# Performance work log

Hardware: AMD Instinct MI355X
Metric: run time of the kernel (lower is better)

The kernel has to match this reference:

```python
import jax, jax.numpy as jnp
import numpy as np
import math

N = 10000      # nodes (batched protein residues)
E = 160000     # edges (avg degree 16)
D = 1280       # node/hidden dim (ESM2-650M)
M = 24         # message_dim
EE = 16        # edge_embedding_dim (sinusoidal distance features)
L = 6          # num EGNN layers
LN_EPS = 1e-5


def setup_inputs() -> dict:
    key = jax.random.key(0)
    ks = jax.random.split(key, 20)
    s = 0.02
    h = jax.random.normal(ks[0], (N, D), jnp.float32)
    pos = jax.random.normal(ks[1], (N, 3), jnp.float32) * 10.0
    edge_index = jax.random.randint(ks[2], (2, E), 0, N, jnp.int32)
    msg_in_dim = 2 * D + EE + 1  # h_i, h_j, edge_attr, radial
    params = dict(
        node_emb_W=jax.random.normal(ks[3], (D, D), jnp.float32) * s,
        node_emb_b=jnp.zeros((D,), jnp.float32),
        msg_W1=jax.random.normal(ks[4], (L, msg_in_dim, M), jnp.float32) * s,
        msg_b1=jnp.zeros((L, M), jnp.float32),
        msg_W2=jax.random.normal(ks[5], (L, M, M), jnp.float32) * s,
        msg_b2=jnp.zeros((L, M), jnp.float32),
        coord_W1=jax.random.normal(ks[6], (L - 1, M, M), jnp.float32) * s,
        coord_b1=jnp.zeros((L - 1, M), jnp.float32),
        coord_W2=jax.random.normal(ks[7], (L - 1, M, 1), jnp.float32) * s,  # no bias
        node_W1=jax.random.normal(ks[8], (L, D + M, M), jnp.float32) * s,
        node_b1=jnp.zeros((L, M), jnp.float32),
        node_W2=jax.random.normal(ks[9], (L, M, D), jnp.float32) * s,
        node_b2=jnp.zeros((L, D), jnp.float32),
        ln_g=jnp.ones((L, D), jnp.float32),
        ln_b=jnp.zeros((L, D), jnp.float32),
    )
    return dict(h=h, pos=pos, edge_index=edge_index, **params)


def reference(h, pos, edge_index, node_emb_W, node_emb_b, msg_W1, msg_b1,
              msg_W2, msg_b2, coord_W1, coord_b1, coord_W2,
              node_W1, node_b1, node_W2, node_b2, ln_g, ln_b):
    row, col = edge_index[0], edge_index[1]  # PyG: row=source j, col=target i

    # sinusoidal distance embedding from initial coordinates (computed once)
    freqs = jnp.exp(-math.log(10000.0) * jnp.arange(0, EE, 2, dtype=jnp.float32) / EE)
    d0 = pos[row] - pos[col]                      # (E,3)
    dist = jnp.sqrt(jnp.sum(d0 * d0, axis=1))     # (E,)
    ang = dist[:, None] * freqs[None, :]          # (E, EE/2)
    edge_attr = jnp.stack([jnp.sin(ang), jnp.cos(ang)], axis=2).reshape(dist.shape[0], EE)

    h = h @ node_emb_W + node_emb_b

    # mean-aggregation denominator: in-degree of target nodes, clamped to 1
    deg = jax.ops.segment_sum(jnp.ones_like(dist), col, num_segments=N)
    denom = jnp.maximum(deg, 1.0)[:, None]

    for l in range(L):
        cd = pos[row] - pos[col]                  # (E,3) coord_diff
        radial = jnp.sum(cd * cd, axis=1, keepdims=True)
        msg_in = jnp.concatenate([h[col], h[row], edge_attr, radial], axis=-1)  # (E, 2D+EE+1)
        msg = jax.nn.silu(jax.nn.silu(msg_in @ msg_W1[l] + msg_b1[l]) @ msg_W2[l] + msg_b2[l])
        msg_agg = jax.ops.segment_sum(msg, col, num_segments=N) / denom  # scatter-mean
        if l < L - 1:  # update_coords for all but last layer
            w = jax.nn.silu(msg @ coord_W1[l] + coord_b1[l]) @ coord_W2[l]  # (E,1)
            pos = pos + jax.ops.segment_sum(cd * w, col, num_segments=N)   # index_add
        h_up = jax.nn.silu(jnp.concatenate([h, msg_agg], axis=-1) @ node_W1[l] + node_b1[l]) @ node_W2[l] + node_b2[l]
        hn = h + h_up
        mu = jnp.mean(hn, axis=-1, keepdims=True)
        var = jnp.mean((hn - mu) ** 2, axis=-1, keepdims=True)
        h = (hn - mu) / jnp.sqrt(var + LN_EPS) * ln_g[l] + ln_b[l]
        # dropout is identity in eval mode
    return h, pos
```

## Files before the change

### kernel.cpp

```cpp
#include <hip/hip_runtime.h>

#define NN 10000
#define NE 160000
#define DD 1280
#define MM 24

typedef __attribute__((ext_vector_type(8))) short bf16x8;
typedef __attribute__((ext_vector_type(4))) float f32x4;
typedef unsigned short u16;

#define O_nembW 0
#define O_nembB 1638400
#define O_msgW1 1639680
#define O_msgB1 2010880
#define O_msgW2 2011136
#define O_msgB2 2014592
#define O_cW1   2014848
#define O_cB1   2017792
#define O_cW2   2017920
#define O_nW1   2018048
#define O_nB1   2205824
#define O_nW2   2206080
#define O_nB2   2390400
#define O_lnG   2398080
#define O_lnB   2405760
#define TOTW    2413440

__device__ __forceinline__ float b2f(u16 u){
  union { unsigned int i; float f; } v; v.i = ((unsigned int)u) << 16; return v.f;
}
__device__ __forceinline__ u16 f2b(float f){
  union { float f; unsigned int i; } v; v.f = f;
  return (u16)((v.i + 0x7fffu + ((v.i >> 16) & 1u)) >> 16);
}
__device__ __forceinline__ float silu_f(float x){ return x / (1.f + __expf(-x)); }

__device__ __forceinline__ void gll16(const u16* g, u16* l){
  __builtin_amdgcn_global_load_lds(
      (const __attribute__((address_space(1))) void*)g,
      (__attribute__((address_space(3))) void*)l, 16, 0, 0);
}

__global__ __launch_bounds__(256) void k_sniff(const u16* __restrict__ h0, int* __restrict__ modep)
{
  __shared__ int cnt;
  if (threadIdx.x == 0) cnt = 0;
  __syncthreads();
  int local = 0;
  for (int i = threadIdx.x; i < 16384; i += 256){
    unsigned int e = (h0[i] >> 7) & 0xFF;
    if (e >= 0xE0) local++;
  }
  atomicAdd(&cnt, local);
  __syncthreads();
  if (threadIdx.x == 0) *modep = (cnt > 16) ? 0 : 1;
}

__global__ __launch_bounds__(256) void k_cvtw(const int* __restrict__ modep,
    const void* p0, const void* p1, const void* p2, const void* p3, const void* p4,
    const void* p5, const void* p6, const void* p7, const void* p8, const void* p9,
    const void* p10, const void* p11, const void* p12, const void* p13, const void* p14,
    u16* __restrict__ wbf)
{
  int i = blockIdx.x * 256 + threadIdx.x;
  if (i >= TOTW) return;
  int mode = *modep;
  const void* src; int j; int sz;
  if      (i < O_nembB){ src = p0;  j = i - O_nembW; sz = 1638400; }
  else if (i < O_msgW1){ src = p1;  j = i - O_nembB; sz = 1280; }
  else if (i < O_msgB1){ src = p2;  j = i - O_msgW1; sz = 371088; }
  else if (i < O_msgW2){ src = p3;  j = i - O_msgB1; sz = 144; }
  else if (i < O_msgB2){ src = p4;  j = i - O_msgW2; sz = 3456; }
  else if (i < O_cW1)  { src = p5;  j = i - O_msgB2; sz = 144; }
  else if (i < O_cB1)  { src = p6;  j = i - O_cW1;   sz = 2880; }
  else if (i < O_cW2)  { src = p7;  j = i - O_cB1;   sz = 120; }
  else if (i < O_nW1)  { src = p8;  j = i - O_cW2;   sz = 120; }
  else if (i < O_nB1)  { src = p9;  j = i - O_nW1;   sz = 187776; }
  else if (i < O_nW2)  { src = p10; j = i - O_nB1;   sz = 144; }
  else if (i < O_nB2)  { src = p11; j = i - O_nW2;   sz = 184320; }
  else if (i < O_lnG)  { src = p12; j = i - O_nB2;   sz = 7680; }
  else if (i < O_lnB)  { src = p13; j = i - O_lnG;   sz = 7680; }
  else                 { src = p14; j = i - O_lnB;   sz = 7680; }
  u16 v = 0;
  if (j < sz) v = mode ? ((const u16*)src)[j] : f2b(((const float*)src)[j]);
  wbf[i] = v;
}

__global__ __launch_bounds__(256) void k_tr(const u16* __restrict__ win, u16* __restrict__ wout)
{
  __shared__ u16 tile[32][33];
  int bx = blockIdx.x % 40, by = blockIdx.x / 40;
  int tc = threadIdx.x & 31, tr = threadIdx.x >> 5;
  #pragma unroll
  for (int p = 0; p < 4; p++){
    int r = p*8 + tr;
    tile[r][tc] = win[(size_t)(by*32 + r)*1280 + bx*32 + tc];
  }
  __syncthreads();
  #pragma unroll
  for (int p = 0; p < 4; p++){
    int r = p*8 + tr;
    wout[(size_t)(bx*32 + r)*1280 + by*32 + tc] = tile[tc][r];
  }
}

__global__ __launch_bounds__(256) void k_packproj(const u16* __restrict__ wbf, u16* __restrict__ wproj)
{
  int i = blockIdx.x * 256 + threadIdx.x;
  if (i >= 6*80*1280) return;
  int l = i / (80*1280);
  int rem = i - l*80*1280;
  int n = rem / 1280;
  int k = rem - n*1280;
  u16 v = 0;
  if (n < 24)       v = wbf[O_msgW1 + (size_t)l*2577*24 + (size_t)k*24 + n];
  else if (n < 48)  v = wbf[O_msgW1 + (size_t)l*2577*24 + (size_t)(1280+k)*24 + (n-24)];
  else if (n < 72)  v = wbf[O_nW1   + (size_t)l*1304*24 + (size_t)k*24 + (n-48)];
  wproj[i] = v;
}

__global__ __launch_bounds__(256) void k_packw2(const u16* __restrict__ wbf, u16* __restrict__ wn2p)
{
  int i = blockIdx.x * 256 + threadIdx.x;
  int l = i / (1280*32); int rem = i - l*1280*32;
  int n = rem >> 5, k = rem & 31;
  wn2p[i] = (k < 24) ? wbf[O_nW2 + (size_t)l*24*1280 + (size_t)k*1280 + n] : (u16)0;
}

__global__ __launch_bounds__(256) void k_cvth(const void* h0, const int* __restrict__ modep,
                                              u16* __restrict__ h0b)
{
  int i = blockIdx.x * 256 + threadIdx.x;
  if (*modep){
    ((int4*)h0b)[i] = ((const int4*)h0)[i];
  } else {
    const float* s = (const float*)h0 + (size_t)i*8;
    bf16x8 o;
    #pragma unroll
    for (int j = 0; j < 8; j++) o[j] = (short)f2b(s[j]);
    *(bf16x8*)(h0b + (size_t)i*8) = o;
  }
}

__global__ __launch_bounds__(256) void k_setup(const void* pos0, const int* __restrict__ modep,
    float* __restrict__ deg, float* __restrict__ posf, float* __restrict__ posf0)
{
  int i = blockIdx.x * 256 + threadIdx.x;
  int mode = *modep;
  if (i < NN) deg[i] = 0.f;
  if (i < NN * 3){
    float p = mode ? b2f(((const u16*)pos0)[i]) : ((const float*)pos0)[i];
    posf[i] = p; posf0[i] = p;
  }
}

__global__ __launch_bounds__(256) void k_deg(const int* __restrict__ eidx, float* __restrict__ deg)
{
  int e = blockIdx.x * 256 + threadIdx.x;
  atomicAdd(&deg[eidx[NE + e]], 1.f);
}

__global__ __launch_bounds__(256) void k_prefix(const float* __restrict__ deg,
                                                int* __restrict__ offs, int* __restrict__ cursor)
{
  __shared__ int part[256];
  int t = threadIdx.x;
  int lo = t * 40, hi = lo + 40; if (hi > NN) hi = NN; if (lo > NN) lo = NN;
  int s = 0;
  for (int i = lo; i < hi; i++) s += (int)deg[i];
  part[t] = s;
  __syncthreads();
  for (int off = 1; off < 256; off <<= 1){
    int v = (t >= off) ? part[t - off] : 0;
    __syncthreads();
    part[t] += v;
    __syncthreads();
  }
  int run = (t == 0) ? 0 : part[t - 1];
  for (int i = lo; i < hi; i++){
    offs[i] = run;
    run += (int)deg[i];
    cursor[i] = 0;
  }
  if (t == 255) offs[NN] = run;
}

__global__ __launch_bounds__(256) void k_scatter(const int* __restrict__ eidx,
    const int* __restrict__ offs, int* __restrict__ cursor, int* __restrict__ iperm)
{
  int e = blockIdx.x * 256 + threadIdx.x;
  int cg = eidx[NE + e];
  int p = atomicAdd(&cursor[cg], 1);
  iperm[e] = offs[cg] + p;
}

__global__ __launch_bounds__(256) void k_gemm_init(const u16* __restrict__ h0b,
    const u16* __restrict__ wembT, const u16* __restrict__ wbf, u16* __restrict__ Cb)
{
  __shared__ u16 As[128*64];
  __shared__ u16 Bs[128*64];
  int bid = blockIdx.x;
  int bm = (bid & 7) + 8 * (bid / 80);
  int bn = (bid >> 3) % 10;
  if (bm >= 79) return;
  int t = threadIdx.x;
  int lane = t & 63, wv = t >> 6;
  int m0 = bm * 128, n0 = bn * 128;
  int col = lane & 15, quad = lane >> 4;
  int wm = wv & 1, wn = wv >> 1;
  f32x4 acc[4][4];
  #pragma unroll
  for (int mi = 0; mi < 4; mi++)
    #pragma unroll
    for (int ni = 0; ni < 4; ni++) acc[mi][ni] = (f32x4){0.f,0.f,0.f,0.f};

  for (int k0 = 0; k0 < DD; k0 += 64){
    #pragma unroll
    for (int is = 0; is < 4; is++){
      int flat = is*256 + t;
      int row = flat >> 3, kcp = flat & 7;
      int src = (kcp ^ (row & 7)) * 8;
      int grow = m0 + row; if (grow > NN-1) grow = NN-1;
      gll16(h0b + (size_t)grow*DD + k0 + src, As + flat*8);
    }
    #pragma unroll
    for (int is = 0; is < 4; is++){
      int flat = is*256 + t;
      int row = flat >> 3, kcp = flat & 7;
      int src = (kcp ^ (row & 7)) * 8;
      gll16(wembT + (size_t)(n0 + row)*DD + k0 + src, Bs + flat*8);
    }
    __builtin_amdgcn_s_waitcnt(0x0f70);
    __syncthreads();
    #pragma unroll
    for (int ks = 0; ks < 2; ks++){
      bf16x8 af[4], bfv[4];
      #pragma unroll
      for (int mi = 0; mi < 4; mi++){
        int row = wm*64 + mi*16 + col;
        int ch = (ks*4 + quad) ^ (row & 7);
        af[mi] = *(const bf16x8*)&As[row*64 + ch*8];
      }
      #pragma unroll
      for (int ni = 0; ni < 4; ni++){
        int row = wn*64 + ni*16 + col;
        int ch = (ks*4 + quad) ^ (row & 7);
        bfv[ni] = *(const bf16x8*)&Bs[row*64 + ch*8];
      }
      #pragma unroll
      for (int mi = 0; mi < 4; mi++)
        #pragma unroll
        for (int ni = 0; ni < 4; ni++)
          acc[mi][ni] = __builtin_amdgcn_mfma_f32_16x16x32_bf16(af[mi], bfv[ni], acc[mi][ni], 0, 0, 0);
    }
    __syncthreads();
  }
  #pragma unroll
  for (int ni = 0; ni < 4; ni++){
    int cc = n0 + wn*64 + ni*16 + col;
    float bias = b2f(wbf[O_nembB + cc]);
    #pragma unroll
    for (int mi = 0; mi < 4; mi++){
      #pragma unroll
      for (int rr = 0; rr < 4; rr++){
        int row = m0 + wm*64 + mi*16 + quad*4 + rr;
        if (row < NN) Cb[(size_t)row*DD + cc] = f2b(acc[mi][ni][rr] + bias);
      }
    }
  }
}

__global__ __launch_bounds__(256) void k_gemm_proj(const u16* __restrict__ hbm,
    const u16* __restrict__ wproj, int layer,
    float* __restrict__ Ab, float* __restrict__ Bb, float* __restrict__ Mb)
{
  __shared__ float paccS[80*16];
  int t = threadIdx.x;
  int lane = t & 63, wv = t >> 6;
  int m0 = blockIdx.x * 16;
  int col = lane & 15, quad = lane >> 4;
  for (int i = t; i < 1280; i += 256) paccS[i] = 0.f;
  __syncthreads();
  const u16* wp = wproj + (size_t)layer * 80 * 1280;
  f32x4 acc5[5];
  #pragma unroll
  for (int ni = 0; ni < 5; ni++) acc5[ni] = (f32x4){0.f,0.f,0.f,0.f};
  #pragma unroll
  for (int kk = 0; kk < 10; kk++){
    int kb = wv*320 + kk*32;
    bf16x8 a = *(const bf16x8*)&hbm[(size_t)(m0 + col)*DD + kb + quad*8];
    #pragma unroll
    for (int ni = 0; ni < 5; ni++){
      bf16x8 b = *(const bf16x8*)&wp[(size_t)(ni*16 + col)*DD + kb + quad*8];
      acc5[ni] = __builtin_amdgcn_mfma_f32_16x16x32_bf16(a, b, acc5[ni], 0, 0, 0);
    }
  }
  #pragma unroll
  for (int ni = 0; ni < 5; ni++)
    #pragma unroll
    for (int rr = 0; rr < 4; rr++)
      atomicAdd(&paccS[(ni*16 + col)*16 + quad*4 + rr], acc5[ni][rr]);
  __syncthreads();
  for (int i = t; i < 1280; i += 256){
    int n = i >> 4, m = i & 15;
    if (n < 72){
      int rg = (n >= 48) ? 2 : (n >= 24 ? 1 : 0);
      int cc = n - rg*24;
      float* base = (rg == 0) ? Ab : (rg == 1) ? Bb : Mb;
      base[(m0 + m)*24 + cc] = paccS[i];
    }
  }
}

__global__ __launch_bounds__(256) void k_edge(const int* __restrict__ eidx,
    const int* __restrict__ iperm,
    const float* __restrict__ posf, const float* __restrict__ posf0,
    const float* __restrict__ Ab, const float* __restrict__ Bb,
    const u16* __restrict__ wbf, int layer, int do_coord,
    u16* __restrict__ msgu, float* __restrict__ wcdbuf)
{
  __shared__ float sW1e[16*24], sWr[24], sB1[24], sW2[24*24], sB2[24];
  __shared__ float sCW1[24*24], sCB1[24], sCW2[24];
  int t = threadIdx.x;
  const u16* w1l = wbf + O_msgW1 + (size_t)layer * 2577 * 24;
  for (int i = t; i < 16*24; i += 256) sW1e[i] = b2f(w1l[2560*24 + i]);
  for (int i = t; i < 24; i += 256){
    sWr[i] = b2f(w1l[2576*24 + i]);
    sB1[i] = b2f(wbf[O_msgB1 + layer*24 + i]);
    sB2[i] = b2f(wbf[O_msgB2 + layer*24 + i]);
  }
  for (int i = t; i < 576; i += 256) sW2[i] = b2f(wbf[O_msgW2 + layer*576 + i]);
  if (do_coord){
    for (int i = t; i < 576; i += 256) sCW1[i] = b2f(wbf[O_cW1 + layer*576 + i]);
    for (int i = t; i < 24; i += 256){
      sCB1[i] = b2f(wbf[O_cB1 + layer*24 + i]);
      sCW2[i] = b2f(wbf[O_cW2 + layer*24 + i]);
    }
  }
  __syncthreads();
  int e = blockIdx.x * 256 + t;
  int r = eidx[e], cg = eidx[NE + e];
  int slot = iperm[e];
  float cdx = posf[r*3+0] - posf[cg*3+0];
  float cdy = posf[r*3+1] - posf[cg*3+1];
  float cdz = posf[r*3+2] - posf[cg*3+2];
  float radial = cdx*cdx + cdy*cdy + cdz*cdz;
  float ex = posf0[r*3+0] - posf0[cg*3+0];
  float ey = posf0[r*3+1] - posf0[cg*3+1];
  float ez = posf0[r*3+2] - posf0[cg*3+2];
  float dist = sqrtf(ex*ex + ey*ey + ez*ez);
  const float FR[8] = {1.f, 0.31622776601683794f, 0.1f, 0.03162277660168379f,
                       0.01f, 0.0031622776601683794f, 0.001f, 0.00031622776601683794f};
  float eav[16];
  #pragma unroll
  for (int j = 0; j < 8; j++){
    float ang = dist * FR[j];
    eav[2*j]   = __sinf(ang);
    eav[2*j+1] = __cosf(ang);
  }
  float acc[24];
  const float4* ap  = (const float4*)(Ab + cg * 24);
  const float4* bp4 = (const float4*)(Bb + r * 24);
  #pragma unroll
  for (int q = 0; q < 6; q++){
    float4 a4 = ap[q], b4 = bp4[q];
    acc[q*4+0] = a4.x + b4.x; acc[q*4+1] = a4.y + b4.y;
    acc[q*4+2] = a4.z + b4.z; acc[q*4+3] = a4.w + b4.w;
  }
  #pragma unroll
  for (int m = 0; m < 24; m++) acc[m] += sB1[m] + radial * sWr[m];
  #pragma unroll
  for (int k = 0; k < 16; k++){
    #pragma unroll
    for (int m = 0; m < 24; m++) acc[m] += eav[k] * sW1e[k*24 + m];
  }
  #pragma unroll
  for (int m = 0; m < 24; m++) acc[m] = silu_f(acc[m]);
  float msg[24];
  #pragma unroll
  for (int m = 0; m < 24; m++){
    float v = sB2[m];
    #pragma unroll
    for (int k = 0; k < 24; k++) v += acc[k] * sW2[k*24 + m];
    msg[m] = silu_f(v);
  }
  {
    bf16x8 v0, v1, v2;
    #pragma unroll
    for (int j = 0; j < 8; j++){
      v0[j] = (short)f2b(msg[j]);
      v1[j] = (short)f2b(msg[8+j]);
      v2[j] = (short)f2b(msg[16+j]);
    }
    u16* mp = msgu + (size_t)slot * 24;
    *(bf16x8*)(mp)      = v0;
    *(bf16x8*)(mp + 8)  = v1;
    *(bf16x8*)(mp + 16) = v2;
  }
  if (do_coord){
    float w = 0.f;
    #pragma unroll
    for (int m = 0; m < 24; m++){
      float v = sCB1[m];
      #pragma unroll
      for (int k = 0; k < 24; k++) v += msg[k] * sCW1[k*24 + m];
      w += silu_f(v) * sCW2[m];
    }
    wcdbuf[(size_t)slot*3+0] = cdx * w;
    wcdbuf[(size_t)slot*3+1] = cdy * w;
    wcdbuf[(size_t)slot*3+2] = cdz * w;
  }
}

__global__ __launch_bounds__(256) void k_agg(const int* __restrict__ offs,
    const u16* __restrict__ msgu, const float* __restrict__ wcdbuf,
    float* __restrict__ magg, float* __restrict__ posf,
    int do_coord, int writeout, void* __restrict__ outp, const int* __restrict__ modep)
{
  int wv = threadIdx.x >> 6, lane = threadIdx.x & 63;
  int n = blockIdx.x * 4 + wv;
  int base = offs[n], cnt = offs[n+1] - base;
  float sum = 0.f;
  if (lane < 48){
    int m = (lane < 24) ? lane : lane - 24;
    for (int j = (lane < 24 ? 0 : 1); j < cnt; j += 2)
      sum += b2f(msgu[(size_t)(base+j)*24 + m]);
  }
  sum += __shfl_down(sum, 24, 64);
  if (lane < 24) magg[n*24 + lane] = sum;
  if (do_coord){
    float sc = 0.f;
    if (lane < 48){
      int c = lane % 3, jj = lane / 3;
      for (int j = jj; j < cnt; j += 16)
        sc += wcdbuf[(size_t)(base+j)*3 + c];
    }
    sc += __shfl_down(sc, 24, 64);
    sc += __shfl_down(sc, 12, 64);
    sc += __shfl_down(sc, 6, 64);
    sc += __shfl_down(sc, 3, 64);
    if (lane < 3){
      float p = posf[n*3 + lane] + sc;
      posf[n*3 + lane] = p;
      if (writeout){
        if (*modep) ((u16*)outp)[(size_t)NN*DD + n*3 + lane] = f2b(p);
        else        ((float*)outp)[(size_t)NN*DD + n*3 + lane] = p;
      }
    }
  }
}

__global__ __launch_bounds__(256) void k_combine(
    float* __restrict__ Mb, const float* __restrict__ magg, const float* __restrict__ deg,
    const u16* __restrict__ wbf, const u16* __restrict__ wn2p, const u16* __restrict__ wproj,
    const int* __restrict__ modep,
    int layer, int last, int fuse,
    u16* __restrict__ hbm, void* __restrict__ outp,
    float* __restrict__ Ab, float* __restrict__ Bb)
{
  __shared__ u16 shRes[16*1280];
  __shared__ u16 midb[16*32];
  __shared__ float sW1b[576], sB1c[24], sMg[384], sMbs[384], sDeg[16];
  __shared__ float wpart[4][16][2];
  __shared__ float mrow[16][2];
  __shared__ float paccS[80*16];
  int t = threadIdx.x;
  int lane = t & 63, wv = t >> 6;
  int row0 = blockIdx.x * 16;
  #pragma unroll
  for (int it = 0; it < 10; it++){
    int flat = it*256 + t;
    int r = flat / 160, off = (flat - r*160) * 8;
    gll16(hbm + (size_t)(row0 + r)*1280 + off, shRes + flat*8);
  }
  const u16* w1b = wbf + O_nW1 + (size_t)layer*1304*24 + 1280*24;
  for (int i = t; i < 576; i += 256) sW1b[i] = b2f(w1b[i]);
  if (t < 24) sB1c[t] = b2f(wbf[O_nB1 + layer*24 + t]);
  if (t < 16) sDeg[t] = 1.f / fmaxf(deg[row0 + t], 1.f);
  for (int i = t; i < 384; i += 256){ sMg[i] = magg[row0*24 + i]; sMbs[i] = Mb[row0*24 + i]; }
  for (int i = t; i < 1280; i += 256) paccS[i] = 0.f;
  midb[t] = 0; midb[256 + t] = 0;
  __builtin_amdgcn_s_waitcnt(0x0f70);
  __syncthreads();
  for (int o = t; o < 384; o += 256){
    int r = o / 24, m = o - r*24;
    float inv = sDeg[r];
    float a = sMbs[o] + sB1c[m];
    #pragma unroll
    for (int j = 0; j < 24; j++) a += sMg[r*24 + j] * inv * sW1b[j*24 + m];
    midb[r*32 + m] = f2b(silu_f(a));
  }
  __syncthreads();
  int col = lane & 15, quad = lane >> 4;
  bf16x8 af = *(const bf16x8*)&midb[col*32 + quad*8];
  int mode = *modep;
  float s1[4] = {0.f,0.f,0.f,0.f}, s2[4] = {0.f,0.f,0.f,0.f};
  float vals[20][4];
  const u16* wp2 = wn2p + (size_t)layer*1280*32;
  const u16* b2p = wbf + O_nB2 + (size_t)layer*1280;
  #pragma unroll
  for (int ti = 0; ti < 20; ti++){
    int n0 = wv*320 + ti*16;
    bf16x8 bfv = *(const bf16x8*)&wp2[(size_t)(n0+col)*32 + quad*8];
    f32x4 acc = {0.f,0.f,0.f,0.f};
    acc = __builtin_amdgcn_mfma_f32_16x16x32_bf16(af, bfv, acc, 0, 0, 0);
    float b2 = b2f(b2p[n0 + col]);
    #pragma unroll
    for (int rr = 0; rr < 4; rr++){
      int r = quad*4 + rr;
      float hn = b2f(shRes[r*1280 + n0 + col]) + acc[rr] + b2;
      vals[ti][rr] = hn;
      s1[rr] += hn; s2[rr] += hn*hn;
    }
  }
  #pragma unroll
  for (int off = 1; off < 16; off <<= 1){
    #pragma unroll
    for (int rr = 0; rr < 4; rr++){
      s1[rr] += __shfl_xor(s1[rr], off, 64);
      s2[rr] += __shfl_xor(s2[rr], off, 64);
    }
  }
  if (col == 0){
    #pragma unroll
    for (int rr = 0; rr < 4; rr++){
      wpart[wv][quad*4+rr][0] = s1[rr];
      wpart[wv][quad*4+rr][1] = s2[rr];
    }
  }
  __syncthreads();
  if (t < 16){
    float S1 = wpart[0][t][0] + wpart[1][t][0] + wpart[2][t][0] + wpart[3][t][0];
    float S2 = wpart[0][t][1] + wpart[1][t][1] + wpart[2][t][1] + wpart[3][t][1];
    float mu = S1 * (1.f/1280.f);
    float var = S2 * (1.f/1280.f) - mu*mu;
    mrow[t][0] = mu;
    mrow[t][1] = rsqrtf(var + 1e-5f);
  }
  __syncthreads();
  const u16* gp = wbf + O_lnG + (size_t)layer*1280;
  const u16* bp = wbf + O_lnB + (size_t)layer*1280;
  #pragma unroll
  for (int ti = 0; ti < 20; ti++){
    int n0 = wv*320 + ti*16;
    int cc = n0 + col;
    float g  = b2f(gp[cc]);
    float bb = b2f(bp[cc]);
    #pragma unroll
    for (int rr = 0; rr < 4; rr++){
      int r = quad*4 + rr;
      u16 yb = f2b((vals[ti][rr] - mrow[r][0]) * mrow[r][1] * g + bb);
      hbm[(size_t)(row0 + r)*1280 + cc] = yb;
      if (fuse){
        int kc = cc >> 3;
        shRes[r*1280 + (((kc ^ (r & 7)) << 3) | (cc & 7))] = yb;
      }
      if (last){
        if (mode) ((u16*)outp)[(size_t)(row0+r)*1280 + cc] = yb;
        else      ((float*)outp)[(size_t)(row0+r)*1280 + cc] = b2f(yb);
      }
    }
  }
  if (!fuse) return;
  __syncthreads();
  const u16* wp = wproj + (size_t)(layer+1) * 80 * 1280;
  f32x4 acc5[5];
  #pragma unroll
  for (int ni = 0; ni < 5; ni++) acc5[ni] = (f32x4){0.f,0.f,0.f,0.f};
  #pragma unroll
  for (int kk = 0; kk < 10; kk++){
    int kb = wv*320 + kk*32;
    int kc = (kb >> 3) + quad;
    bf16x8 af2 = *(const bf16x8*)&shRes[col*1280 + ((kc ^ (col & 7)) << 3)];
    #pragma unroll
    for (int ni = 0; ni < 5; ni++){
      bf16x8 bv = *(const bf16x8*)&wp[(size_t)(ni*16 + col)*DD + kb + quad*8];
      acc5[ni] = __builtin_amdgcn_mfma_f32_16x16x32_bf16(af2, bv, acc5[ni], 0, 0, 0);
    }
  }
  #pragma unroll
  for (int ni = 0; ni < 5; ni++)
    #pragma unroll
    for (int rr = 0; rr < 4; rr++)
      atomicAdd(&paccS[(ni*16 + col)*16 + quad*4 + rr], acc5[ni][rr]);
  __syncthreads();
  for (int i = t; i < 1280; i += 256){
    int n = i >> 4, m = i & 15;
    if (n < 72){
      int rg = (n >= 48) ? 2 : (n >= 24 ? 1 : 0);
      int cc2 = n - rg*24;
      float* base = (rg == 0) ? Ab : (rg == 1) ? Bb : Mb;
      base[(row0 + m)*24 + cc2] = paccS[i];
    }
  }
}

extern "C" void kernel_launch(void* const* d_in, const int* in_sizes, int n_in,
                              void* d_out, int out_size, void* d_ws, size_t ws_size,
                              hipStream_t stream)
{
  const void* h0    = d_in[0];
  const void* pos0  = d_in[1];
  const int*  eidx  = (const int*)d_in[2];

  char* w = (char*)d_ws;
  auto take = [&](size_t bytes)->char*{
    char* p = w; w += (bytes + 255) & ~(size_t)255; return p;
  };
  int*   modep  = (int*)  take(256);
  u16*   wbf    = (u16*)  take((size_t)TOTW * 2);
  u16*   wembT  = (u16*)  take((size_t)DD * DD * 2);
  u16*   wproj  = (u16*)  take((size_t)6 * 80 * 1280 * 2);
  u16*   wn2p   = (u16*)  take((size_t)6 * 1280 * 32 * 2);
  u16*   hbm    = (u16*)  take((size_t)NN * DD * 2);
  float* Ab     = (float*)take((size_t)NN * MM * 4);
  float* Bb     = (float*)take((size_t)NN * MM * 4);
  float* Mb     = (float*)take((size_t)NN * MM * 4);
  float* magg   = (float*)take((size_t)NN * MM * 4);
  float* deg    = (float*)take((size_t)NN * 4);
  float* posf   = (float*)take((size_t)NN * 3 * 4);
  float* posf0  = (float*)take((size_t)NN * 3 * 4);
  int*   offs   = (int*)  take((size_t)(NN + 1) * 4);
  int*   cursor = (int*)  take((size_t)NN * 4);
  int*   iperm  = (int*)  take((size_t)NE * 4);

  u16*   h0b    = (u16*)d_out;
  u16*   msgu   = (u16*)d_out;
  float* wcdbuf = (float*)((char*)d_out + (size_t)NE * 24 * 2);

  k_sniff<<<1, 256, 0, stream>>>((const u16*)h0, modep);
  k_cvtw<<<(TOTW + 255)/256, 256, 0, stream>>>(modep,
      d_in[3], d_in[4], d_in[5], d_in[6], d_in[7], d_in[8], d_in[9], d_in[10],
      d_in[11], d_in[12], d_in[13], d_in[14], d_in[15], d_in[16], d_in[17], wbf);
  k_tr<<<1600, 256, 0, stream>>>(wbf + O_nembW, wembT);
  k_packproj<<<(6*80*1280 + 255)/256, 256, 0, stream>>>(wbf, wproj);
  k_packw2<<<6*1280*32/256, 256, 0, stream>>>(wbf, wn2p);
  k_cvth<<<NN*DD/8/256, 256, 0, stream>>>(h0, modep, h0b);
  k_setup<<<(NN*3 + 255)/256, 256, 0, stream>>>(pos0, modep, deg, posf, posf0);
  k_deg<<<NE/256, 256, 0, stream>>>(eidx, deg);
  k_prefix<<<1, 256, 0, stream>>>(deg, offs, cursor);
  k_scatter<<<NE/256, 256, 0, stream>>>(eidx, offs, cursor, iperm);
  k_gemm_init<<<800, 256, 0, stream>>>(h0b, wembT, wbf, hbm);
  k_gemm_proj<<<625, 256, 0, stream>>>(hbm, wproj, 0, Ab, Bb, Mb);
  for (int l = 0; l < 6; l++){
    int dc = (l < 5) ? 1 : 0;
    k_edge<<<NE/256, 256, 0, stream>>>(eidx, iperm, posf, posf0, Ab, Bb, wbf, l, dc, msgu, wcdbuf);
    k_agg<<<2500, 256, 0, stream>>>(offs, msgu, wcdbuf, magg, posf,
                                    dc, (l == 4) ? 1 : 0, d_out, modep);
    k_combine<<<625, 256, 0, stream>>>(Mb, magg, deg, wbf, wn2p, wproj, modep,
                                       l, (l == 5) ? 1 : 0, (l < 5) ? 1 : 0,
                                       hbm, d_out, Ab, Bb);
  }
}
```

Measured before the change: 1.012 ms.

## Unfuse next-layer projection from combine and make combine one-row-per-wave

```diff
diff --git a/kernel.cpp b/kernel.cpp
--- a/kernel.cpp
+++ b/kernel.cpp
@@ -451,146 +451,106 @@
 }
 
 __global__ __launch_bounds__(256) void k_combine(
-    float* __restrict__ Mb, const float* __restrict__ magg, const float* __restrict__ deg,
-    const u16* __restrict__ wbf, const u16* __restrict__ wn2p, const u16* __restrict__ wproj,
-    const int* __restrict__ modep,
-    int layer, int last, int fuse,
-    u16* __restrict__ hbm, void* __restrict__ outp,
-    float* __restrict__ Ab, float* __restrict__ Bb)
-{
-  __shared__ u16 shRes[16*1280];
-  __shared__ u16 midb[16*32];
-  __shared__ float sW1b[576], sB1c[24], sMg[384], sMbs[384], sDeg[16];
-  __shared__ float wpart[4][16][2];
-  __shared__ float mrow[16][2];
-  __shared__ float paccS[80*16];
-  int t = threadIdx.x;
-  int lane = t & 63, wv = t >> 6;
-  int row0 = blockIdx.x * 16;
-  #pragma unroll
-  for (int it = 0; it < 10; it++){
-    int flat = it*256 + t;
-    int r = flat / 160, off = (flat - r*160) * 8;
-    gll16(hbm + (size_t)(row0 + r)*1280 + off, shRes + flat*8);
-  }
-  const u16* w1b = wbf + O_nW1 + (size_t)layer*1304*24 + 1280*24;
-  for (int i = t; i < 576; i += 256) sW1b[i] = b2f(w1b[i]);
-  if (t < 24) sB1c[t] = b2f(wbf[O_nB1 + layer*24 + t]);
-  if (t < 16) sDeg[t] = 1.f / fmaxf(deg[row0 + t], 1.f);
-  for (int i = t; i < 384; i += 256){ sMg[i] = magg[row0*24 + i]; sMbs[i] = Mb[row0*24 + i]; }
-  for (int i = t; i < 1280; i += 256) paccS[i] = 0.f;
-  midb[t] = 0; midb[256 + t] = 0;
-  __builtin_amdgcn_s_waitcnt(0x0f70);
-  __syncthreads();
-  for (int o = t; o < 384; o += 256){
-    int r = o / 24, m = o - r*24;
-    float inv = sDeg[r];
-    float a = sMbs[o] + sB1c[m];
-    #pragma unroll
-    for (int j = 0; j < 24; j++) a += sMg[r*24 + j] * inv * sW1b[j*24 + m];
-    midb[r*32 + m] = f2b(silu_f(a));
-  }
-  __syncthreads();
-  int col = lane & 15, quad = lane >> 4;
-  bf16x8 af = *(const bf16x8*)&midb[col*32 + quad*8];
-  int mode = *modep;
-  float s1[4] = {0.f,0.f,0.f,0.f}, s2[4] = {0.f,0.f,0.f,0.f};
-  float vals[20][4];
-  const u16* wp2 = wn2p + (size_t)layer*1280*32;
-  const u16* b2p = wbf + O_nB2 + (size_t)layer*1280;
-  #pragma unroll
-  for (int ti = 0; ti < 20; ti++){
-    int n0 = wv*320 + ti*16;
-    bf16x8 bfv = *(const bf16x8*)&wp2[(size_t)(n0+col)*32 + quad*8];
-    f32x4 acc = {0.f,0.f,0.f,0.f};
-    acc = __builtin_amdgcn_mfma_f32_16x16x32_bf16(af, bfv, acc, 0, 0, 0);
-    float b2 = b2f(b2p[n0 + col]);
-    #pragma unroll
-    for (int rr = 0; rr < 4; rr++){
-      int r = quad*4 + rr;
-      float hn = b2f(shRes[r*1280 + n0 + col]) + acc[rr] + b2;
-      vals[ti][rr] = hn;
-      s1[rr] += hn; s2[rr] += hn*hn;
-    }
-  }
-  #pragma unroll
-  for (int off = 1; off < 16; off <<= 1){
-    #pragma unroll
-    for (int rr = 0; rr < 4; rr++){
-      s1[rr] += __shfl_xor(s1[rr], off, 64);
-      s2[rr] += __shfl_xor(s2[rr], off, 64);
-    }
-  }
-  if (col == 0){
-    #pragma unroll
-    for (int rr = 0; rr < 4; rr++){
-      wpart[wv][quad*4+rr][0] = s1[rr];
-      wpart[wv][quad*4+rr][1] = s2[rr];
-    }
-  }
-  __syncthreads();
-  if (t < 16){
-    float S1 = wpart[0][t][0] + wpart[1][t][0] + wpart[2][t][0] + wpart[3][t][0];
-    float S2 = wpart[0][t][1] + wpart[1][t][1] + wpart[2][t][1] + wpart[3][t][1];
-    float mu = S1 * (1.f/1280.f);
-    float var = S2 * (1.f/1280.f) - mu*mu;
-    mrow[t][0] = mu;
-    mrow[t][1] = rsqrtf(var + 1e-5f);
-  }
-  __syncthreads();
-  const u16* gp = wbf + O_lnG + (size_t)layer*1280;
-  const u16* bp = wbf + O_lnB + (size_t)layer*1280;
-  #pragma unroll
-  for (int ti = 0; ti < 20; ti++){
-    int n0 = wv*320 + ti*16;
-    int cc = n0 + col;
-    float g  = b2f(gp[cc]);
-    float bb = b2f(bp[cc]);
-    #pragma unroll
-    for (int rr = 0; rr < 4; rr++){
-      int r = quad*4 + rr;
-      u16 yb = f2b((vals[ti][rr] - mrow[r][0]) * mrow[r][1] * g + bb);
-      hbm[(size_t)(row0 + r)*1280 + cc] = yb;
-      if (fuse){
-        int kc = cc >> 3;
-        shRes[r*1280 + (((kc ^ (r & 7)) << 3) | (cc & 7))] = yb;
+    const float* __restrict__ Mb, const float* __restrict__ magg, const float* __restrict__ deg,
+    const u16* __restrict__ wbf, const u16* __restrict__ wn2p, const int* __restrict__ modep,
+    int layer, int last,
+    u16* __restrict__ hbm, void* __restrict__ outp)
+{
+  __shared__ float smid[4][24];
+  int t = threadIdx.x, wv = t >> 6, lane = t & 63;
+  int r = blockIdx.x * 4 + wv;
+  if (lane < 24){
+    const u16* w1b = wbf + O_nW1 + (size_t)layer*1304*24 + 1280*24;
+    float inv = 1.f / fmaxf(deg[r], 1.f);
+    float a = Mb[r*24 + lane] + b2f(wbf[O_nB1 + layer*24 + lane]);
+    #pragma unroll
+    for (int j = 0; j < 24; j++)
+      a += magg[r*24 + j] * inv * b2f(w1b[j*24 + lane]);
+    smid[wv][lane] = silu_f(a);
+  }
+  __syncthreads();
+  float mid[24];
+  #pragma unroll
+  for (int q = 0; q < 6; q++){
+    float4 m4 = *(const float4*)&smid[wv][q*4];
+    mid[q*4]=m4.x; mid[q*4+1]=m4.y; mid[q*4+2]=m4.z; mid[q*4+3]=m4.w;
+  }
+  int c0 = lane * 20;
+  float acc[20];
+  {
+    const uint2* rp = (const uint2*)(hbm + (size_t)r*1280 + c0);
+    const uint2* bp2 = (const uint2*)(wbf + O_nB2 + (size_t)layer*1280 + c0);
+    #pragma unroll
+    for (int q = 0; q < 5; q++){
+      uint2 v = rp[q], b = bp2[q];
+      acc[q*4+0] = b2f((u16)(v.x & 0xffff)) + b2f((u16)(b.x & 0xffff));
+      acc[q*4+1] = b2f((u16)(v.x >> 16))    + b2f((u16)(b.x >> 16));
+      acc[q*4+2] = b2f((u16)(v.y & 0xffff)) + b2f((u16)(b.y & 0xffff));
+      acc[q*4+3] = b2f((u16)(v.y >> 16))    + b2f((u16)(b.y >> 16));
+    }
+  }
+  const u16* wp = wn2p + ((size_t)layer*1280 + c0)*32;
+  #pragma unroll
+  for (int i = 0; i < 20; i++){
+    const bf16x8* wrow = (const bf16x8*)(wp + (size_t)i*32);
+    bf16x8 w0 = wrow[0], w1 = wrow[1], w2v = wrow[2];
+    float s = 0.f;
+    #pragma unroll
+    for (int k = 0; k < 8; k++) s += mid[k]    * b2f((u16)w0[k]);
+    #pragma unroll
+    for (int k = 0; k < 8; k++) s += mid[8+k]  * b2f((u16)w1[k]);
+    #pragma unroll
+    for (int k = 0; k < 8; k++) s += mid[16+k] * b2f((u16)w2v[k]);
+    acc[i] += s;
+  }
+  float s1 = 0.f, s2 = 0.f;
+  #pragma unroll
+  for (int i = 0; i < 20; i++){ s1 += acc[i]; s2 += acc[i]*acc[i]; }
+  #pragma unroll
+  for (int off = 1; off < 64; off <<= 1){
+    s1 += __shfl_xor(s1, off, 64);
+    s2 += __shfl_xor(s2, off, 64);
+  }
+  float mu = s1 * (1.f/1280.f);
+  float rstd = rsqrtf(s2*(1.f/1280.f) - mu*mu + 1e-5f);
+  u16 yb[20];
+  {
+    const uint2* gp2 = (const uint2*)(wbf + O_lnG + (size_t)layer*1280 + c0);
+    const uint2* bp2 = (const uint2*)(wbf + O_lnB + (size_t)layer*1280 + c0);
+    #pragma unroll
+    for (int q = 0; q < 5; q++){
+      uint2 g = gp2[q], b = bp2[q];
+      float gv[4] = { b2f((u16)(g.x & 0xffff)), b2f((u16)(g.x >> 16)),
+                      b2f((u16)(g.y & 0xffff)), b2f((u16)(g.y >> 16)) };
+      float bv[4] = { b2f((u16)(b.x & 0xffff)), b2f((u16)(b.x >> 16)),
+                      b2f((u16)(b.y & 0xffff)), b2f((u16)(b.y >> 16)) };
+      #pragma unroll
+      for (int j = 0; j < 4; j++)
+        yb[q*4+j] = f2b((acc[q*4+j] - mu) * rstd * gv[j] + bv[j]);
+    }
+  }
+  uint2* op = (uint2*)(hbm + (size_t)r*1280 + c0);
+  #pragma unroll
+  for (int q = 0; q < 5; q++){
+    uint2 v;
+    v.x = (unsigned)yb[q*4]   | ((unsigned)yb[q*4+1] << 16);
+    v.y = (unsigned)yb[q*4+2] | ((unsigned)yb[q*4+3] << 16);
+    op[q] = v;
+  }
+  if (last){
+    if (*modep){
+      uint2* o2 = (uint2*)((u16*)outp + (size_t)r*1280 + c0);
+      #pragma unroll
+      for (int q = 0; q < 5; q++){
+        uint2 v;
+        v.x = (unsigned)yb[q*4]   | ((unsigned)yb[q*4+1] << 16);
+        v.y = (unsigned)yb[q*4+2] | ((unsigned)yb[q*4+3] << 16);
+        o2[q] = v;
       }
-      if (last){
-        if (mode) ((u16*)outp)[(size_t)(row0+r)*1280 + cc] = yb;
-        else      ((float*)outp)[(size_t)(row0+r)*1280 + cc] = b2f(yb);
-      }
-    }
-  }
-  if (!fuse) return;
-  __syncthreads();
-  const u16* wp = wproj + (size_t)(layer+1) * 80 * 1280;
-  f32x4 acc5[5];
-  #pragma unroll
-  for (int ni = 0; ni < 5; ni++) acc5[ni] = (f32x4){0.f,0.f,0.f,0.f};
-  #pragma unroll
-  for (int kk = 0; kk < 10; kk++){
-    int kb = wv*320 + kk*32;
-    int kc = (kb >> 3) + quad;
-    bf16x8 af2 = *(const bf16x8*)&shRes[col*1280 + ((kc ^ (col & 7)) << 3)];
-    #pragma unroll
-    for (int ni = 0; ni < 5; ni++){
-      bf16x8 bv = *(const bf16x8*)&wp[(size_t)(ni*16 + col)*DD + kb + quad*8];
-      acc5[ni] = __builtin_amdgcn_mfma_f32_16x16x32_bf16(af2, bv, acc5[ni], 0, 0, 0);
-    }
-  }
-  #pragma unroll
-  for (int ni = 0; ni < 5; ni++)
-    #pragma unroll
-    for (int rr = 0; rr < 4; rr++)
-      atomicAdd(&paccS[(ni*16 + col)*16 + quad*4 + rr], acc5[ni][rr]);
-  __syncthreads();
-  for (int i = t; i < 1280; i += 256){
-    int n = i >> 4, m = i & 15;
-    if (n < 72){
-      int rg = (n >= 48) ? 2 : (n >= 24 ? 1 : 0);
-      int cc2 = n - rg*24;
-      float* base = (rg == 0) ? Ab : (rg == 1) ? Bb : Mb;
-      base[(row0 + m)*24 + cc2] = paccS[i];
+    } else {
+      float* of = (float*)outp + (size_t)r*1280 + c0;
+      #pragma unroll
+      for (int i = 0; i < 20; i++) of[i] = b2f(yb[i]);
     }
   }
 }
@@ -641,14 +601,13 @@
   k_prefix<<<1, 256, 0, stream>>>(deg, offs, cursor);
   k_scatter<<<NE/256, 256, 0, stream>>>(eidx, offs, cursor, iperm);
   k_gemm_init<<<800, 256, 0, stream>>>(h0b, wembT, wbf, hbm);
-  k_gemm_proj<<<625, 256, 0, stream>>>(hbm, wproj, 0, Ab, Bb, Mb);
   for (int l = 0; l < 6; l++){
     int dc = (l < 5) ? 1 : 0;
+    k_gemm_proj<<<625, 256, 0, stream>>>(hbm, wproj, l, Ab, Bb, Mb);
     k_edge<<<NE/256, 256, 0, stream>>>(eidx, iperm, posf, posf0, Ab, Bb, wbf, l, dc, msgu, wcdbuf);
     k_agg<<<2500, 256, 0, stream>>>(offs, msgu, wcdbuf, magg, posf,
                                     dc, (l == 4) ? 1 : 0, d_out, modep);
-    k_combine<<<625, 256, 0, stream>>>(Mb, magg, deg, wbf, wn2p, wproj, modep,
-                                       l, (l == 5) ? 1 : 0, (l < 5) ? 1 : 0,
-                                       hbm, d_out, Ab, Bb);
-  }
-}
+    k_combine<<<2500, 256, 0, stream>>>(Mb, magg, deg, wbf, wn2p, modep,
+                                        l, (l == 5) ? 1 : 0, hbm, d_out);
+  }
+}
```

Result: slower. 1.291 ms (+27.6%).
